# Kernel tuning notes

Measured on AMD Instinct MI355X. Metric: run time of the kernel, lower is better.

## Reference

```python
import jax, jax.numpy as jnp
import numpy as np

N, IN_CHN, MDIM, ATT_D, NUM_CLS = 100000, 1024, 512, 128, 2
NUM_GROUP, INST_PER_GROUP = 8, 4
GROUP_SIZE = N // NUM_GROUP


def setup_inputs() -> dict:
    key = jax.random.key(0)
    ks = jax.random.split(key, 8)
    def w(k, shape, fan):
        return (jax.random.normal(k, shape, jnp.float32) / np.sqrt(fan)).astype(jnp.float32)
    return {
        "index_chunk_list": jax.random.randint(ks[0], (NUM_GROUP, GROUP_SIZE), 0, N),
        "tfeat_tensor": jax.random.normal(ks[1], (N, IN_CHN), jnp.float32),
        # DimReduction: Linear(1024 -> mDim) + ReLU (numLayer_Res = 0)
        "W1": w(ks[2], (MDIM, IN_CHN), IN_CHN), "b1": jnp.zeros((MDIM,), jnp.float32),
        # Attention: Linear(mDim -> 128), tanh, Linear(128 -> 1)
        "Wa1": w(ks[3], (ATT_D, MDIM), MDIM), "ba1": jnp.zeros((ATT_D,), jnp.float32),
        "Wa2": w(ks[4], (1, ATT_D), ATT_D), "ba2": jnp.zeros((1,), jnp.float32),
        # Classifier_1fc: Linear(mDim -> num_cls)  (dropout=0 -> identity)
        "Wc": w(ks[5], (NUM_CLS, MDIM), MDIM), "bc": jnp.zeros((NUM_CLS,), jnp.float32),
    }


def _group_forward(idx, tfeat, W1, b1, Wa1, ba1, Wa2, ba2, Wc, bc):
    # idx: [S] instance indices for one pseudo-bag
    sub = jnp.take(tfeat, idx, axis=0)                       # [S, in_chn]  gather
    mid = jax.nn.relu(sub @ W1.T + b1)                       # [S, m]       DimReduction
    a = jnp.tanh(mid @ Wa1.T + ba1) @ Wa2.T + ba2            # [S, 1]       Attention logits
    a = jax.nn.softmax(a[:, 0], axis=0)                      # [S]          softmax over instances
    att = mid * a[:, None]                                   # [S, m]       einsum('ns,n->ns')
    bag = att.sum(axis=0)                                    # [m]          attention-weighted sum
    pred = bag @ Wc.T + bc                                    # [C]          bag-level logits
    # get_cam_1d: per-instance logits from classifier weight only (no bias)
    cam = jax.nn.softmax(att @ Wc.T, axis=1)                  # [S, C]
    order = jnp.argsort(-cam[:, -1])                          # descending sort on last-class prob
    topk = jnp.concatenate([order[:INST_PER_GROUP], order[-INST_PER_GROUP:]])
    maxmin = jnp.take(mid, topk, axis=0)                      # [2k, m]  MaxMinS distill feats
    return pred, maxmin


def reference(index_chunk_list, tfeat_tensor, W1, b1, Wa1, ba1, Wa2, ba2, Wc, bc):
    f = jax.vmap(_group_forward, in_axes=(0,) + (None,) * 9)
    slide_sub_preds, slide_pseudo_feat = f(index_chunk_list, tfeat_tensor,
                                           W1, b1, Wa1, ba1, Wa2, ba2, Wc, bc)
    # [numGroup, num_cls], [numGroup, 2*instance_per_group, mDim]
    return slide_sub_preds, slide_pseudo_feat
```

## Files before the change

kernel.cpp:

```cpp
#include <hip/hip_runtime.h>
#include <stdint.h>

#define N_TOT 100000
#define IN_CHN 1024
#define MDIM 512
#define ATT_D 128
#define NUM_GROUP 8
#define GROUP_SIZE 12500
#define LDST 72
#define SEGR 98

typedef __bf16 bf16x8 __attribute__((ext_vector_type(8)));
typedef float f32x4 __attribute__((ext_vector_type(4)));
typedef unsigned short u16x8 __attribute__((ext_vector_type(8)));

__device__ __forceinline__ unsigned short f2bf(float x){
  union { float f; unsigned u; } v; v.f = x;
  unsigned r = v.u + 0x7fffu + ((v.u >> 16) & 1u);
  return (unsigned short)(r >> 16);
}
__device__ __forceinline__ float bf2f(unsigned short h){
  union { unsigned u; float f; } v; v.u = ((unsigned)h) << 16; return v.f;
}
__device__ __forceinline__ void gload16(const void* g, void* l){
  __builtin_amdgcn_global_load_lds(
      (const __attribute__((address_space(1))) unsigned int*)g,
      (__attribute__((address_space(3))) unsigned int*)l, 16, 0, 0);
}

__global__ __launch_bounds__(256) void kconv(const float* __restrict__ W1,
                                             const float* __restrict__ Wa1,
                                             unsigned short* __restrict__ W1b,
                                             unsigned short* __restrict__ Wa1b){
  int i = blockIdx.x * 256 + threadIdx.x;
  if (i < MDIM * IN_CHN) W1b[i] = f2bf(W1[i]);
  else {
    int j = i - MDIM * IN_CHN;
    if (j < ATT_D * MDIM) Wa1b[j] = f2bf(Wa1[j]);
  }
}

__global__ __launch_bounds__(256) void kgemm_mid(const int* __restrict__ idxf,
                                                 const float* __restrict__ tfeat,
                                                 const unsigned short* __restrict__ W1b,
                                                 const float* __restrict__ b1,
                                                 unsigned short* __restrict__ midb,
                                                 int base){
  __shared__ alignas(16) float Af0[128 * 32];
  __shared__ alignas(16) float Af1[128 * 32];
  __shared__ alignas(16) unsigned short Bsm[128 * 64];
  __shared__ int gsm[128];
  int tid = threadIdx.x;
  int bidg = blockIdx.x + base;
  int tile = (bidg & 7) * 391 + (bidg >> 3);
  int bn = tile & 3, bm = tile >> 2;
  int m0 = bm * 128, n0 = bn * 128;
  if (tid < 128){ int r = m0 + tid; gsm[tid] = idxf[r < N_TOT ? r : 0]; }
  __syncthreads();

  int w = tid >> 6, l = tid & 63;
  int l16 = tid & 15, hi = (tid >> 4) & 3;
  int wm = tid >> 7, wn = (tid >> 6) & 1;

  const float* asrc[4];
  const unsigned short* bsrc[4];
  int adsto[4], bdsto[4];
  int scw = (l & 7) ^ (l >> 3);
  #pragma unroll
  for (int q = 0; q < 4; q++){
    int rowl = q * 32 + w * 8 + (l >> 3);
    asrc[q] = tfeat + (size_t)gsm[rowl] * IN_CHN + scw * 4;
    bsrc[q] = W1b + (size_t)(n0 + rowl) * IN_CHN + scw * 8;
    adsto[q] = (q * 32 + w * 8) * 32;
    bdsto[q] = (q * 32 + w * 8) * 64;
  }

  f32x4 acc[4][4];
  #pragma unroll
  for (int a = 0; a < 4; a++)
    #pragma unroll
    for (int b = 0; b < 4; b++) acc[a][b] = (f32x4){0.f, 0.f, 0.f, 0.f};

  int r7 = l16 & 7;

  for (int s = 0; s < 16; s++){
    __syncthreads();
    #pragma unroll
    for (int q = 0; q < 4; q++){
      gload16(asrc[q] + s * 64,      &Af0[adsto[q]]);
      gload16(asrc[q] + s * 64 + 32, &Af1[adsto[q]]);
      gload16(bsrc[q] + s * 64,      &Bsm[bdsto[q]]);
    }
    __syncthreads();

    #pragma unroll
    for (int ks = 0; ks < 2; ks++){
      const float* At = ks ? Af1 : Af0;
      bf16x8 af[4], bfr[4];
      #pragma unroll
      for (int a = 0; a < 4; a++){
        int row = wm * 64 + a * 16 + l16;
        f32x4 lo  = *(const f32x4*)&At[row * 32 + (((2 * hi) ^ r7) << 2)];
        f32x4 hi4 = *(const f32x4*)&At[row * 32 + (((2 * hi + 1) ^ r7) << 2)];
        bf16x8 pk;
        pk[0] = (__bf16)lo[0]; pk[1] = (__bf16)lo[1]; pk[2] = (__bf16)lo[2]; pk[3] = (__bf16)lo[3];
        pk[4] = (__bf16)hi4[0]; pk[5] = (__bf16)hi4[1]; pk[6] = (__bf16)hi4[2]; pk[7] = (__bf16)hi4[3];
        af[a] = pk;
      }
      #pragma unroll
      for (int b = 0; b < 4; b++){
        int row = wn * 64 + b * 16 + l16;
        bfr[b] = *(const bf16x8*)&Bsm[row * 64 + (((ks * 4 + hi) ^ r7) << 3)];
      }
      #pragma unroll
      for (int a = 0; a < 4; a++)
        #pragma unroll
        for (int b = 0; b < 4; b++)
          acc[a][b] = __builtin_amdgcn_mfma_f32_16x16x32_bf16(af[a], bfr[b], acc[a][b], 0, 0, 0);
    }
  }

  #pragma unroll
  for (int b = 0; b < 4; b++){
    int col = n0 + wn * 64 + b * 16 + l16;
    float bias = b1[col];
    #pragma unroll
    for (int a = 0; a < 4; a++){
      int rbase = m0 + wm * 64 + a * 16 + hi * 4;
      #pragma unroll
      for (int q = 0; q < 4; q++){
        int row = rbase + q;
        if (row < N_TOT){
          float v = acc[a][b][q] + bias;
          midb[(size_t)row * MDIM + col] = f2bf(fmaxf(v, 0.f));
        }
      }
    }
  }
}

__global__ __launch_bounds__(256) void kattn(const unsigned short* __restrict__ midb,
                                             const unsigned short* __restrict__ Wa1b,
                                             const float* __restrict__ ba1,
                                             const float* __restrict__ Wa2,
                                             const float* __restrict__ ba2,
                                             const float* __restrict__ Wc,
                                             float* __restrict__ lv,
                                             float* __restrict__ tv){
  __shared__ alignas(16) unsigned short Asm[128 * LDST];
  __shared__ alignas(16) unsigned short Bsm[128 * LDST];
  __shared__ float dsh[512];
  __shared__ float part[128][2];
  int tid = threadIdx.x;
  int m0 = blockIdx.x * 128;
  for (int i = tid; i < 512; i += 256) dsh[i] = Wc[512 + i] - Wc[i];

  int lane8 = tid & 7, rq = tid >> 3;
  const unsigned short *asrc[4], *bsrc[4];
  unsigned short *adst[4], *bdst[4];
  #pragma unroll
  for (int p = 0; p < 4; p++){
    int r = p * 32 + rq;
    int rowc = m0 + r; if (rowc > N_TOT - 1) rowc = N_TOT - 1;
    asrc[p] = midb + (size_t)rowc * MDIM + lane8 * 8;
    bsrc[p] = Wa1b + (size_t)r * MDIM + lane8 * 8;
    adst[p] = &Asm[r * LDST + lane8 * 8];
    bdst[p] = &Bsm[r * LDST + lane8 * 8];
  }
  int l16 = tid & 15, hi = (tid >> 4) & 3;
  int wm = tid >> 7, wn = (tid >> 6) & 1;
  f32x4 acc[4][4];
  #pragma unroll
  for (int a = 0; a < 4; a++)
    #pragma unroll
    for (int b = 0; b < 4; b++) acc[a][b] = (f32x4){0.f, 0.f, 0.f, 0.f};
  float tpart[4] = {0.f, 0.f, 0.f, 0.f};

  for (int s = 0; s < 8; s++){
    __syncthreads();
    #pragma unroll
    for (int p = 0; p < 4; p++){
      u16x8 av = *(const u16x8*)(asrc[p] + s * 64);
      *(u16x8*)adst[p] = av;
      *(u16x8*)bdst[p] = *(const u16x8*)(bsrc[p] + s * 64);
      #pragma unroll
      for (int e = 0; e < 8; e++)
        tpart[p] += bf2f((unsigned short)av[e]) * dsh[s * 64 + lane8 * 8 + e];
    }
    __syncthreads();
    #pragma unroll
    for (int ks = 0; ks < 2; ks++){
      int off = (ks * 4 + hi) * 8;
      bf16x8 af[4], bfr[4];
      #pragma unroll
      for (int a = 0; a < 4; a++){ int row = wm * 64 + a * 16 + l16; af[a] = *(const bf16x8*)&Asm[row * LDST + off]; }
      #pragma unroll
      for (int b = 0; b < 4; b++){ int col = wn * 64 + b * 16 + l16; bfr[b] = *(const bf16x8*)&Bsm[col * LDST + off]; }
      #pragma unroll
      for (int a = 0; a < 4; a++)
        #pragma unroll
        for (int b = 0; b < 4; b++)
          acc[a][b] = __builtin_amdgcn_mfma_f32_16x16x32_bf16(af[a], bfr[b], acc[a][b], 0, 0, 0);
    }
  }
  #pragma unroll
  for (int p = 0; p < 4; p++){
    float t = tpart[p];
    t += __shfl_xor(t, 1); t += __shfl_xor(t, 2); t += __shfl_xor(t, 4);
    if (lane8 == 0){
      int row = m0 + p * 32 + rq;
      if (row < N_TOT) tv[row] = t;
    }
  }
  #pragma unroll
  for (int a = 0; a < 4; a++){
    #pragma unroll
    for (int q = 0; q < 4; q++){
      float v = 0.f;
      #pragma unroll
      for (int b = 0; b < 4; b++){
        int col = wn * 64 + b * 16 + l16;
        v += tanhf(acc[a][b][q] + ba1[col]) * Wa2[col];
      }
      #pragma unroll
      for (int off = 1; off < 16; off <<= 1) v += __shfl_xor(v, off);
      if (l16 == 0) part[wm * 64 + a * 16 + hi * 4 + q][wn] = v;
    }
  }
  __syncthreads();
  if (tid < 128){
    int row = m0 + tid;
    if (row < N_TOT) lv[row] = part[tid][0] + part[tid][1] + ba2[0];
  }
}

__global__ __launch_bounds__(256) void kselect(const float* __restrict__ lv,
                                               const float* __restrict__ tv,
                                               float* __restrict__ maxlw, float* __restrict__ Zw,
                                               int* __restrict__ cand,
                                               float* __restrict__ w){
  __shared__ float keys[GROUP_SIZE];
  __shared__ float candk[4096];
  __shared__ int   candi[4096];
  __shared__ float rk[256];
  __shared__ int ri[256];
  __shared__ int rs[256];
  __shared__ float sbc;
  int g = blockIdx.x, tid = threadIdx.x;
  const float* lg = lv + (size_t)g * GROUP_SIZE;
  const float* tg = tv + (size_t)g * GROUP_SIZE;

  float mx = -1e30f;
  for (int i = tid; i < GROUP_SIZE; i += 256) mx = fmaxf(mx, lg[i]);
  rk[tid] = mx; __syncthreads();
  for (int s = 128; s > 0; s >>= 1){ if (tid < s) rk[tid] = fmaxf(rk[tid], rk[tid + s]); __syncthreads(); }
  if (tid == 0) sbc = rk[0];
  __syncthreads();
  float maxl = sbc;

  float z = 0.f;
  for (int i = tid; i < GROUP_SIZE; i += 256){
    float ez = expf(lg[i] - maxl);
    z += ez;
    keys[i] = ez * tg[i];
  }
  rk[tid] = z; __syncthreads();
  for (int s = 128; s > 0; s >>= 1){ if (tid < s) rk[tid] += rk[tid + s]; __syncthreads(); }
  if (tid == 0){ maxlw[g] = maxl; Zw[g] = rk[0]; }
  __syncthreads();
  float invZ = 1.0f / rk[0];
  for (int i = tid; i < GROUP_SIZE; i += 256)
    w[(size_t)g * GROUP_SIZE + i] = expf(lg[i] - maxl) * invZ;
  __syncthreads();

  {
    float tk[16]; int tix[16];
    #pragma unroll
    for (int j = 0; j < 16; j++){ tk[j] = -1e30f; tix[j] = 0x7fffffff; }
    for (int i = tid; i < GROUP_SIZE; i += 256){
      float ck = keys[i];
      if (ck > tk[15]){
        int ci = i;
        #pragma unroll
        for (int j = 0; j < 16; j++){
          bool ins = ck > tk[j];
          float nk = ins ? ck : tk[j]; int ni = ins ? ci : tix[j];
          float ok = ins ? tk[j] : ck; int oi = ins ? tix[j] : ci;
          tk[j] = nk; tix[j] = ni; ck = ok; ci = oi;
        }
      }
    }
    #pragma unroll
    for (int j = 0; j < 16; j++){ candk[tid * 16 + j] = tk[j]; candi[tid * 16 + j] = tix[j]; }
  }
  __syncthreads();
  for (int it = 0; it < 16; it++){
    float bk = -1e30f; int bi = 0x7fffffff; int bs = -1;
    for (int jj = tid; jj < 4096; jj += 256){
      float k = candk[jj]; int ix = candi[jj];
      if (k > bk || (k == bk && ix < bi)){ bk = k; bi = ix; bs = jj; }
    }
    rk[tid] = bk; ri[tid] = bi; rs[tid] = bs; __syncthreads();
    for (int s = 128; s > 0; s >>= 1){
      if (tid < s){
        if (rk[tid + s] > rk[tid] || (rk[tid + s] == rk[tid] && ri[tid + s] < ri[tid])){
          rk[tid] = rk[tid + s]; ri[tid] = ri[tid + s]; rs[tid] = rs[tid + s];
        }
      }
      __syncthreads();
    }
    if (tid == 0){ cand[g * 32 + it] = ri[0]; candk[rs[0]] = -1e30f; }
    __syncthreads();
  }

  {
    float tk[16]; int tix[16];
    #pragma unroll
    for (int j = 0; j < 16; j++){ tk[j] = 1e30f; tix[j] = -1; }
    for (int i = tid; i < GROUP_SIZE; i += 256){
      float ck = keys[i];
      if (ck <= tk[15]){
        int ci = i;
        #pragma unroll
        for (int j = 0; j < 16; j++){
          bool ins = ck <= tk[j];
          float nk = ins ? ck : tk[j]; int ni = ins ? ci : tix[j];
          float ok = ins ? tk[j] : ck; int oi = ins ? tix[j] : ci;
          tk[j] = nk; tix[j] = ni; ck = ok; ci = oi;
        }
      }
    }
    #pragma unroll
    for (int j = 0; j < 16; j++){ candk[tid * 16 + j] = tk[j]; candi[tid * 16 + j] = tix[j]; }
  }
  __syncthreads();
  for (int it = 0; it < 16; it++){
    float bk = 1e30f; int bi = -1; int bs = -1;
    for (int jj = tid; jj < 4096; jj += 256){
      float k = candk[jj]; int ix = candi[jj];
      if (k < bk || (k == bk && ix > bi)){ bk = k; bi = ix; bs = jj; }
    }
    rk[tid] = bk; ri[tid] = bi; rs[tid] = bs; __syncthreads();
    for (int s = 128; s > 0; s >>= 1){
      if (tid < s){
        if (rk[tid + s] < rk[tid] || (rk[tid + s] == rk[tid] && ri[tid + s] > ri[tid])){
          rk[tid] = rk[tid + s]; ri[tid] = ri[tid + s]; rs[tid] = rs[tid + s];
        }
      }
      __syncthreads();
    }
    if (tid == 0){ cand[g * 32 + 16 + it] = ri[0]; candk[rs[0]] = 1e30f; }
    __syncthreads();
  }
}

__global__ __launch_bounds__(256) void kexact(const int* __restrict__ idxf,
                                              const float* __restrict__ tfeat,
                                              const float* __restrict__ W1,
                                              const float* __restrict__ b1,
                                              const float* __restrict__ Wa1,
                                              const float* __restrict__ ba1,
                                              const float* __restrict__ Wa2,
                                              const float* __restrict__ ba2,
                                              const float* __restrict__ Wc,
                                              const int* __restrict__ cand,
                                              const float* __restrict__ maxlw,
                                              float* __restrict__ emid, float* __restrict__ ekey){
  __shared__ float subs[1024];
  __shared__ float midc[512];
  __shared__ float hs[128];
  __shared__ float red[256];
  __shared__ float tsh;
  int bid = blockIdx.x; int g = bid >> 5, c = bid & 31; int tid = threadIdx.x;
  int s = cand[g * 32 + c];
  int inst = idxf[g * GROUP_SIZE + s];
  ((float4*)subs)[tid] = ((const float4*)(tfeat + (size_t)inst * IN_CHN))[tid];
  __syncthreads();

  float a0 = b1[tid], a1 = b1[tid + 256];
  const float4* w0 = (const float4*)(W1 + (size_t)tid * IN_CHN);
  const float4* w1 = (const float4*)(W1 + ((size_t)tid + 256) * IN_CHN);
  const float4* s4 = (const float4*)subs;
  #pragma unroll 4
  for (int k = 0; k < 256; k++){
    float4 sv = s4[k], wva = w0[k], wvb = w1[k];
    a0 += sv.x * wva.x + sv.y * wva.y + sv.z * wva.z + sv.w * wva.w;
    a1 += sv.x * wvb.x + sv.y * wvb.y + sv.z * wvb.z + sv.w * wvb.w;
  }
  a0 = fmaxf(a0, 0.f); a1 = fmaxf(a1, 0.f);
  midc[tid] = a0; midc[tid + 256] = a1;
  size_t eo = (size_t)(g * 32 + c) * MDIM;
  emid[eo + tid] = a0; emid[eo + tid + 256] = a1;
  __syncthreads();

  if (tid < 128){
    const float4* wr = (const float4*)(Wa1 + (size_t)tid * MDIM);
    const float4* m4 = (const float4*)midc;
    float h = ba1[tid];
    #pragma unroll 4
    for (int j = 0; j < 128; j++){
      float4 mv = m4[j], wv = wr[j];
      h += mv.x * wv.x + mv.y * wv.y + mv.z * wv.z + mv.w * wv.w;
    }
    hs[tid] = tanhf(h) * Wa2[tid];
  }
  __syncthreads();

  float tp = midc[tid] * (Wc[512 + tid] - Wc[tid]) + midc[tid + 256] * (Wc[768 + tid] - Wc[256 + tid]);
  red[tid] = tp; __syncthreads();
  for (int st = 128; st > 0; st >>= 1){ if (tid < st) red[tid] += red[tid + st]; __syncthreads(); }
  if (tid == 0) tsh = red[0];
  __syncthreads();
  red[tid] = (tid < 128) ? hs[tid] : 0.f; __syncthreads();
  for (int st = 128; st > 0; st >>= 1){ if (tid < st) red[tid] += red[tid + st]; __syncthreads(); }
  if (tid == 0){
    float lval = red[0] + ba2[0];
    ekey[g * 32 + c] = expf(lval - maxlw[g]) * tsh;
  }
}

__global__ __launch_bounds__(256) void kbag(const unsigned short* __restrict__ midb,
                                            const float* __restrict__ w,
                                            float* __restrict__ bagp){
  __shared__ float wl[SEGR];
  int g = blockIdx.x >> 7, seg = blockIdx.x & 127, tid = threadIdx.x;
  int i0 = seg * SEGR;
  int nr = GROUP_SIZE - i0; if (nr > SEGR) nr = SEGR;
  size_t base = (size_t)g * GROUP_SIZE;
  if (tid < nr) wl[tid] = w[base + i0 + tid];
  __syncthreads();
  float a0 = 0.f, a1 = 0.f;
  const unsigned short* mp = midb + (base + i0) * MDIM + 2 * tid;
  int i = 0;
  for (; i + 2 <= nr; i += 2){
    unsigned pk0 = *(const unsigned*)(mp + (size_t)i * MDIM);
    unsigned pk1 = *(const unsigned*)(mp + (size_t)(i + 1) * MDIM);
    float w0 = wl[i], w1 = wl[i + 1];
    a0 += w0 * bf2f((unsigned short)(pk0 & 0xffff)) + w1 * bf2f((unsigned short)(pk1 & 0xffff));
    a1 += w0 * bf2f((unsigned short)(pk0 >> 16)) + w1 * bf2f((unsigned short)(pk1 >> 16));
  }
  if (i < nr){
    unsigned pk0 = *(const unsigned*)(mp + (size_t)i * MDIM);
    float w0 = wl[i];
    a0 += w0 * bf2f((unsigned short)(pk0 & 0xffff));
    a1 += w0 * bf2f((unsigned short)(pk0 >> 16));
  }
  float* dst = bagp + (size_t)blockIdx.x * MDIM + 2 * tid;
  dst[0] = a0; dst[1] = a1;
}

__global__ __launch_bounds__(256) void kfinal(const float* __restrict__ bagp,
                                              const float* __restrict__ Wc,
                                              const float* __restrict__ bc,
                                              const float* __restrict__ emid,
                                              const float* __restrict__ ekey,
                                              const int* __restrict__ cand,
                                              float* __restrict__ out){
  __shared__ float k32[32];
  __shared__ int s32[32];
  __shared__ int ordv[32];
  __shared__ float r0[256], r1[256];
  int g = blockIdx.x, tid = threadIdx.x;
  if (tid < 32){ k32[tid] = ekey[g * 32 + tid]; s32[tid] = cand[g * 32 + tid]; }
  __syncthreads();
  if (tid == 0){
    unsigned used = 0;
    for (int a = 0; a < 32; a++){
      int best = -1;
      for (int b = 0; b < 32; b++){
        if ((used >> b) & 1u) continue;
        if (best < 0 || k32[b] > k32[best] || (k32[b] == k32[best] && s32[b] < s32[best])) best = b;
      }
      used |= 1u << best;
      ordv[a] = best;
    }
  }
  float p0 = 0.f, p1 = 0.f;
  for (int j = tid; j < 512; j += 256){
    float bv = 0.f;
    for (int s2 = 0; s2 < 128; s2++) bv += bagp[(size_t)(g * 128 + s2) * MDIM + j];
    p0 += bv * Wc[j];
    p1 += bv * Wc[512 + j];
  }
  r0[tid] = p0; r1[tid] = p1; __syncthreads();
  for (int s = 128; s > 0; s >>= 1){ if (tid < s){ r0[tid] += r0[tid + s]; r1[tid] += r1[tid + s]; } __syncthreads(); }
  if (tid == 0){
    out[g * 2 + 0] = r0[0] + bc[0];
    out[g * 2 + 1] = r1[0] + bc[1];
  }
  __syncthreads();
  for (int p = 0; p < 8; p++){
    int cc = ordv[p < 4 ? p : 24 + p];
    const float* src = emid + (size_t)(g * 32 + cc) * MDIM;
    float* dst = out + 16 + (size_t)(g * 8 + p) * MDIM;
    for (int j = tid; j < 512; j += 256) dst[j] = src[j];
  }
}

extern "C" void kernel_launch(void* const* d_in, const int* in_sizes, int n_in,
                              void* d_out, int out_size, void* d_ws, size_t ws_size,
                              hipStream_t stream){
  const int*   idxf = (const int*)d_in[0];
  const float* tfeat= (const float*)d_in[1];
  const float* W1   = (const float*)d_in[2];
  const float* b1   = (const float*)d_in[3];
  const float* Wa1  = (const float*)d_in[4];
  const float* ba1  = (const float*)d_in[5];
  const float* Wa2  = (const float*)d_in[6];
  const float* ba2  = (const float*)d_in[7];
  const float* Wc   = (const float*)d_in[8];
  const float* bc   = (const float*)d_in[9];
  float* out = (float*)d_out;
  (void)in_sizes; (void)n_in; (void)out_size; (void)ws_size;

  char* ws = (char*)d_ws;
  size_t off = 0;
  auto alloc = [&](size_t bytes){ void* p = ws + off; off += (bytes + 255) & ~(size_t)255; return p; };
  float* lv    = (float*)alloc((size_t)N_TOT * 4);
  float* tv    = (float*)alloc((size_t)N_TOT * 4);
  float* maxlw = (float*)alloc(NUM_GROUP * 4);
  float* Zw    = (float*)alloc(NUM_GROUP * 4);
  int*   cand  = (int*)alloc(NUM_GROUP * 32 * 4);
  float* ekey  = (float*)alloc(NUM_GROUP * 32 * 4);
  float* emid  = (float*)alloc((size_t)NUM_GROUP * 32 * MDIM * 4);
  float* bagp  = (float*)alloc((size_t)NUM_GROUP * 128 * MDIM * 4);
  unsigned short* W1b  = (unsigned short*)alloc((size_t)MDIM * IN_CHN * 2);
  unsigned short* Wa1b = (unsigned short*)alloc((size_t)ATT_D * MDIM * 2);
  unsigned short* midb = (unsigned short*)alloc((size_t)N_TOT * MDIM * 2);
  float* w = tv;

  kconv<<<2304, 256, 0, stream>>>(W1, Wa1, W1b, Wa1b);
  kgemm_mid<<<1564, 256, 0, stream>>>(idxf, tfeat, W1b, b1, midb, 0);
  kgemm_mid<<<1564, 256, 0, stream>>>(idxf, tfeat, W1b, b1, midb, 1564);
  kattn<<<782, 256, 0, stream>>>(midb, Wa1b, ba1, Wa2, ba2, Wc, lv, tv);
  kselect<<<8, 256, 0, stream>>>(lv, tv, maxlw, Zw, cand, w);
  kexact<<<256, 256, 0, stream>>>(idxf, tfeat, W1, b1, Wa1, ba1, Wa2, ba2, Wc, cand, maxlw, emid, ekey);
  kbag<<<1024, 256, 0, stream>>>(midb, w, bagp);
  kfinal<<<8, 256, 0, stream>>>(bagp, Wc, bc, emid, ekey, cand, out);
}
```

Before: 684.7 us.

## Use direct global-to-LDS loads with XOR swizzle in attention kernel; merge GEMM launches

The attention kernel now stages midb and Wa1 tiles with global_load_lds 16-byte direct copies into an XOR-swizzled 64-wide LDS layout. Before, each tile went through registers into a padded layout. The class-difference dot product (tv) is now computed by reading back from LDS after the MFMA step, not from the loaded registers. The two split kgemm_mid launches are merged into one launch of 3128 blocks, removing a launch boundary. One risk is that the last block's rows are no longer clamped to N_TOT, so rows past the end of midb may be read, which can go out of bounds.

Result: faster. 656.8 us (-4.1%).

```diff
diff --git a/kernel.cpp b/kernel.cpp
--- a/kernel.cpp
+++ b/kernel.cpp
@@ -7,7 +7,6 @@
 #define ATT_D 128
 #define NUM_GROUP 8
 #define GROUP_SIZE 12500
-#define LDST 72
 #define SEGR 98
 
 typedef __bf16 bf16x8 __attribute__((ext_vector_type(8)));
@@ -44,14 +43,13 @@
                                                  const float* __restrict__ tfeat,
                                                  const unsigned short* __restrict__ W1b,
                                                  const float* __restrict__ b1,
-                                                 unsigned short* __restrict__ midb,
-                                                 int base){
+                                                 unsigned short* __restrict__ midb){
   __shared__ alignas(16) float Af0[128 * 32];
   __shared__ alignas(16) float Af1[128 * 32];
   __shared__ alignas(16) unsigned short Bsm[128 * 64];
   __shared__ int gsm[128];
   int tid = threadIdx.x;
-  int bidg = blockIdx.x + base;
+  int bidg = blockIdx.x;
   int tile = (bidg & 7) * 391 + (bidg >> 3);
   int bn = tile & 3, bm = tile >> 2;
   int m0 = bm * 128, n0 = bn * 128;
@@ -147,70 +145,80 @@
                                              const float* __restrict__ Wc,
                                              float* __restrict__ lv,
                                              float* __restrict__ tv){
-  __shared__ alignas(16) unsigned short Asm[128 * LDST];
-  __shared__ alignas(16) unsigned short Bsm[128 * LDST];
+  __shared__ alignas(16) unsigned short Asm[128 * 64];
+  __shared__ alignas(16) unsigned short Bsm[128 * 64];
   __shared__ float dsh[512];
   __shared__ float part[128][2];
   int tid = threadIdx.x;
   int m0 = blockIdx.x * 128;
   for (int i = tid; i < 512; i += 256) dsh[i] = Wc[512 + i] - Wc[i];
 
-  int lane8 = tid & 7, rq = tid >> 3;
-  const unsigned short *asrc[4], *bsrc[4];
-  unsigned short *adst[4], *bdst[4];
-  #pragma unroll
-  for (int p = 0; p < 4; p++){
-    int r = p * 32 + rq;
-    int rowc = m0 + r; if (rowc > N_TOT - 1) rowc = N_TOT - 1;
-    asrc[p] = midb + (size_t)rowc * MDIM + lane8 * 8;
-    bsrc[p] = Wa1b + (size_t)r * MDIM + lane8 * 8;
-    adst[p] = &Asm[r * LDST + lane8 * 8];
-    bdst[p] = &Bsm[r * LDST + lane8 * 8];
-  }
+  int w = tid >> 6, l = tid & 63;
   int l16 = tid & 15, hi = (tid >> 4) & 3;
   int wm = tid >> 7, wn = (tid >> 6) & 1;
+  int scw = (l & 7) ^ (l >> 3);
+
+  const unsigned short *asrc[4], *bsrc[4];
+  int dsto[4];
+  #pragma unroll
+  for (int q = 0; q < 4; q++){
+    int rowl = q * 32 + w * 8 + (l >> 3);
+    asrc[q] = midb + (size_t)(m0 + rowl) * MDIM + scw * 8;
+    bsrc[q] = Wa1b + (size_t)rowl * MDIM + scw * 8;
+    dsto[q] = (q * 32 + w * 8) * 64;
+  }
+
   f32x4 acc[4][4];
   #pragma unroll
   for (int a = 0; a < 4; a++)
     #pragma unroll
     for (int b = 0; b < 4; b++) acc[a][b] = (f32x4){0.f, 0.f, 0.f, 0.f};
-  float tpart[4] = {0.f, 0.f, 0.f, 0.f};
+  int r7 = l16 & 7;
+
+  int rt = tid >> 1, kh = tid & 1;
+  int rt7 = rt & 7;
+  float t = 0.f;
 
   for (int s = 0; s < 8; s++){
     __syncthreads();
     #pragma unroll
-    for (int p = 0; p < 4; p++){
-      u16x8 av = *(const u16x8*)(asrc[p] + s * 64);
-      *(u16x8*)adst[p] = av;
-      *(u16x8*)bdst[p] = *(const u16x8*)(bsrc[p] + s * 64);
-      #pragma unroll
-      for (int e = 0; e < 8; e++)
-        tpart[p] += bf2f((unsigned short)av[e]) * dsh[s * 64 + lane8 * 8 + e];
+    for (int q = 0; q < 4; q++){
+      gload16(asrc[q] + s * 64, &Asm[dsto[q]]);
+      gload16(bsrc[q] + s * 64, &Bsm[dsto[q]]);
     }
     __syncthreads();
     #pragma unroll
     for (int ks = 0; ks < 2; ks++){
-      int off = (ks * 4 + hi) * 8;
       bf16x8 af[4], bfr[4];
       #pragma unroll
-      for (int a = 0; a < 4; a++){ int row = wm * 64 + a * 16 + l16; af[a] = *(const bf16x8*)&Asm[row * LDST + off]; }
-      #pragma unroll
-      for (int b = 0; b < 4; b++){ int col = wn * 64 + b * 16 + l16; bfr[b] = *(const bf16x8*)&Bsm[col * LDST + off]; }
+      for (int a = 0; a < 4; a++){
+        int row = wm * 64 + a * 16 + l16;
+        af[a] = *(const bf16x8*)&Asm[row * 64 + (((ks * 4 + hi) ^ r7) << 3)];
+      }
+      #pragma unroll
+      for (int b = 0; b < 4; b++){
+        int row = wn * 64 + b * 16 + l16;
+        bfr[b] = *(const bf16x8*)&Bsm[row * 64 + (((ks * 4 + hi) ^ r7) << 3)];
+      }
       #pragma unroll
       for (int a = 0; a < 4; a++)
         #pragma unroll
         for (int b = 0; b < 4; b++)
           acc[a][b] = __builtin_amdgcn_mfma_f32_16x16x32_bf16(af[a], bfr[b], acc[a][b], 0, 0, 0);
     }
-  }
-  #pragma unroll
-  for (int p = 0; p < 4; p++){
-    float t = tpart[p];
-    t += __shfl_xor(t, 1); t += __shfl_xor(t, 2); t += __shfl_xor(t, 4);
-    if (lane8 == 0){
-      int row = m0 + p * 32 + rq;
-      if (row < N_TOT) tv[row] = t;
-    }
+    #pragma unroll
+    for (int j = 0; j < 4; j++){
+      int gc = kh * 4 + j;
+      u16x8 v = *(const u16x8*)&Asm[rt * 64 + ((gc ^ rt7) << 3)];
+      int kb = s * 64 + gc * 8;
+      #pragma unroll
+      for (int e = 0; e < 8; e++) t += bf2f((unsigned short)v[e]) * dsh[kb + e];
+    }
+  }
+  t += __shfl_xor(t, 1);
+  if (kh == 0){
+    int row = m0 + rt;
+    if (row < N_TOT) tv[row] = t;
   }
   #pragma unroll
   for (int a = 0; a < 4; a++){
@@ -530,8 +538,7 @@
   float* w = tv;
 
   kconv<<<2304, 256, 0, stream>>>(W1, Wa1, W1b, Wa1b);
-  kgemm_mid<<<1564, 256, 0, stream>>>(idxf, tfeat, W1b, b1, midb, 0);
-  kgemm_mid<<<1564, 256, 0, stream>>>(idxf, tfeat, W1b, b1, midb, 1564);
+  kgemm_mid<<<3128, 256, 0, stream>>>(idxf, tfeat, W1b, b1, midb);
   kattn<<<782, 256, 0, stream>>>(midb, Wa1b, ba1, Wa2, ba2, Wc, lv, tv);
   kselect<<<8, 256, 0, stream>>>(lv, tv, maxlw, Zw, cand, w);
   kexact<<<256, 256, 0, stream>>>(idxf, tfeat, W1, b1, Wa1, ba1, Wa2, ba2, Wc, cand, maxlw, emid, ekey);
```
